# Kernel optimization log

Measured on AMD Instinct MI355X. Metric: run time of the kernel, lower is better.

The kernel has to match this reference:

```python
import jax, jax.numpy as jnp
import numpy as np

N = 100000      # nodes
E = 3200000     # edges
F_IN = 128      # dataset.num_features
H = 64          # hidden_channels
H2 = 32         # hidden_channels_2 (H//2); hidden_channels_3 unused by the module
C5 = 256        # 2 * num_features
NC = 6          # num_classes


def setup_inputs() -> dict:
    key = jax.random.key(0)
    ks = jax.random.split(key, 24)

    def w(k, fi, fo):
        return jax.random.normal(k, (fi, fo), jnp.float32) / np.float32(np.sqrt(fi))

    inp = {
        "x": jax.random.normal(ks[0], (N, F_IN), jnp.float32),
        "edge_index": jax.random.randint(ks[1], (2, E), 0, N, dtype=jnp.int32),
        "batch": jnp.zeros((N,), jnp.int32),
        # GCNConv weights/biases (conv_i: x @ W then normalized aggregation + b)
        "W1": w(ks[2], F_IN, H),  "b1": jnp.zeros((H,), jnp.float32),
        "W2": w(ks[3], H, H),     "b2": jnp.zeros((H,), jnp.float32),
        "W3": w(ks[4], H, H2),    "b3": jnp.zeros((H2,), jnp.float32),
        "W4": w(ks[5], H2, H2),   "b4": jnp.zeros((H2,), jnp.float32),
        "W5": w(ks[6], H2, C5),   "b5": jnp.zeros((C5,), jnp.float32),
        # Linear layers
        "Wl1": w(ks[7], C5, 24),  "bl1": jnp.zeros((24,), jnp.float32),
        "Wl2": w(ks[8], 24, 18),  "bl2": jnp.zeros((18,), jnp.float32),
        "Wl3": w(ks[9], 18, 12),  "bl3": jnp.zeros((12,), jnp.float32),
        "Wc":  w(ks[10], 24, NC), "bc": jnp.zeros((NC,), jnp.float32),
    }
    return inp


def reference(x, edge_index, batch,
              W1, b1, W2, b2, W3, b3, W4, b4, W5, b5,
              Wl1, bl1, Wl2, bl2, Wl3, bl3, Wc, bc):
    # --- GCN normalization (PyG GCNConv: add self loops, sym norm) ---
    loops = jnp.arange(N, dtype=edge_index.dtype)
    src = jnp.concatenate([edge_index[0], loops])   # message sources (x_j)
    dst = jnp.concatenate([edge_index[1], loops])   # aggregation targets
    deg = jax.ops.segment_sum(jnp.ones_like(dst, jnp.float32), dst, num_segments=N)
    dinv = jnp.where(deg > 0, jax.lax.rsqrt(jnp.maximum(deg, 1.0)), 0.0)
    norm = (dinv[src] * dinv[dst])[:, None]         # [E+N, 1]

    def gcn(h, W, b):
        m = (h @ W)[src] * norm
        return jax.ops.segment_sum(m, dst, num_segments=N) + b

    h = jnp.tanh(gcn(x, W1, b1))
    h = jnp.tanh(gcn(h, W2, b2))
    h = jnp.tanh(gcn(h, W3, b3))
    h = jnp.tanh(gcn(h, W4, b4))
    h = jnp.tanh(gcn(h, W5, b5))
    h = jnp.tanh(h @ Wl1 + bl1)
    h = jnp.tanh(h @ Wl2 + bl2)
    h = jnp.tanh(h @ Wl3 + bl3)                      # [N, 12]
    e = jnp.concatenate([h[edge_index[0]], h[edge_index[1]]], axis=1)  # [E, 24]
    out = e @ Wc + bc                                # [E, NC]
    return (out, e)
```

## Files before the change

### kernel.cpp

```cpp
#include <hip/hip_runtime.h>

constexpr int BKT_SHIFT = 7;
constexpr int NBKT_PAD  = 1024;
constexpr int CHUNK     = 8192;
constexpr int MAXSEG    = 6144;

__global__ __launch_bounds__(256) void k1_hist(const int* __restrict__ dst,
                                               int* __restrict__ Hist, int ne) {
    __shared__ int lh[NBKT_PAD];
    for (int i = threadIdx.x; i < NBKT_PAD; i += 256) lh[i] = 0;
    __syncthreads();
    int base = blockIdx.x * CHUNK;
    int lim = min(CHUNK, ne - base);
    for (int i = threadIdx.x; i < lim; i += 256)
        atomicAdd(&lh[dst[base + i] >> BKT_SHIFT], 1);
    __syncthreads();
    for (int i = threadIdx.x; i < NBKT_PAD; i += 256)
        Hist[(size_t)blockIdx.x * NBKT_PAD + i] = lh[i];
}

__global__ __launch_bounds__(1024) void k2_scan(int* __restrict__ Hist,
                                                int* __restrict__ bktBase,
                                                int* __restrict__ row_ptrN, int nblk) {
    __shared__ int wsums[16];
    int t = threadIdx.x, wave = t >> 6, lane = t & 63;
    int tot = 0;
    for (int blk = 0; blk < nblk; ++blk) tot += Hist[(size_t)blk * NBKT_PAD + t];
    int x = tot;
    #pragma unroll
    for (int off = 1; off < 64; off <<= 1) {
        int y = __shfl_up(x, off, 64);
        if (lane >= off) x += y;
    }
    if (lane == 63) wsums[wave] = x;
    __syncthreads();
    if (t < 16) {
        int w = wsums[t];
        #pragma unroll
        for (int off = 1; off < 16; off <<= 1) {
            int y = __shfl_up(w, off, 64);
            if (t >= off) w += y;
        }
        wsums[t] = w;
    }
    __syncthreads();
    int excl = (wave ? wsums[wave - 1] : 0) + (x - tot);
    bktBase[t] = excl;
    if (t == 1023) { bktBase[1024] = excl + tot; *row_ptrN = excl + tot; }
    int run = excl;
    for (int blk = 0; blk < nblk; ++blk) {
        size_t idx = (size_t)blk * NBKT_PAD + t;
        int v = Hist[idx];
        Hist[idx] = run;
        run += v;
    }
}

__global__ __launch_bounds__(256) void k3_partition(const int* __restrict__ src,
                                                    const int* __restrict__ dst,
                                                    const int* __restrict__ Hist,
                                                    int* __restrict__ srcS,
                                                    int* __restrict__ dstS, int ne) {
    __shared__ int cur[NBKT_PAD];
    for (int i = threadIdx.x; i < NBKT_PAD; i += 256)
        cur[i] = Hist[(size_t)blockIdx.x * NBKT_PAD + i];
    __syncthreads();
    int base = blockIdx.x * CHUNK;
    int lim = min(CHUNK, ne - base);
    for (int i = threadIdx.x; i < lim; i += 256) {
        int d = dst[base + i];
        int s = src[base + i];
        int pos = atomicAdd(&cur[d >> BKT_SHIFT], 1);
        srcS[pos] = s;
        dstS[pos] = d;
    }
}

__global__ __launch_bounds__(256) void k4_csr(const int* __restrict__ srcS,
                                              const int* __restrict__ dstS,
                                              const int* __restrict__ bktBase,
                                              int* __restrict__ col_idx,
                                              int* __restrict__ row_ptr,
                                              float* __restrict__ dinv, int n) {
    __shared__ int hist[128];
    __shared__ int rbase[128];
    __shared__ int cur[128];
    __shared__ int stage[MAXSEG];
    int b = blockIdx.x;
    int segs = bktBase[b], sege = bktBase[b + 1];
    int seglen = sege - segs;
    int node0 = b << BKT_SHIFT;
    int nloc = min(128, n - node0);
    int t = threadIdx.x;
    if (t < 128) hist[t] = 0;
    __syncthreads();
    for (int i = t; i < seglen; i += 256)
        atomicAdd(&hist[dstS[segs + i] - node0], 1);
    __syncthreads();
    if (t < 64) {
        int a0 = hist[2 * t], a1 = hist[2 * t + 1];
        int pair = a0 + a1;
        int x = pair;
        #pragma unroll
        for (int off = 1; off < 64; off <<= 1) {
            int y = __shfl_up(x, off, 64);
            if (t >= off) x += y;
        }
        int excl = x - pair;
        rbase[2 * t] = excl;       rbase[2 * t + 1] = excl + a0;
        cur[2 * t]   = excl;       cur[2 * t + 1]   = excl + a0;
    }
    __syncthreads();
    if (seglen <= MAXSEG) {
        for (int i = t; i < seglen; i += 256) {
            int d = dstS[segs + i] - node0;
            int pos = atomicAdd(&cur[d], 1);
            stage[pos] = srcS[segs + i];
        }
        __syncthreads();
        for (int i = t; i < seglen; i += 256)
            col_idx[segs + i] = stage[i];
    } else {
        for (int i = t; i < seglen; i += 256) {
            int d = dstS[segs + i] - node0;
            int pos = atomicAdd(&cur[d], 1);
            col_idx[segs + pos] = srcS[segs + i];
        }
    }
    if (t < nloc) {
        row_ptr[node0 + t] = segs + rbase[t];
        dinv[node0 + t] = 1.0f / sqrtf((float)(hist[t] + 1));
    }
}

template<int K, int FOUT, int EPI, int RT>
__global__ __launch_bounds__(256) void gemm_tiled(const float* __restrict__ X,
        const float* __restrict__ W, const float* __restrict__ bias,
        const float* __restrict__ dinv, float* __restrict__ Y, int nrows) {
    __shared__ float Wl[K * FOUT];
    __shared__ float Xs[RT * K];
    int tid = threadIdx.x;
    const float4* Wg4 = (const float4*)W;
    float4* Wl4 = (float4*)Wl;
    for (int i = tid; i < K * FOUT / 4; i += 256) Wl4[i] = Wg4[i];
    int row0 = blockIdx.x * RT;
    int nr = min(RT, nrows - row0);
    if constexpr ((K & 3) == 0) {
        const float4* Xg4 = (const float4*)(X + (size_t)row0 * K);
        float4* Xs4 = (float4*)Xs;
        int lim = nr * (K / 4);
        for (int i = tid; i < lim; i += 256) Xs4[i] = Xg4[i];
    } else {
        const float* Xg = X + (size_t)row0 * K;
        int lim = nr * K;
        for (int i = tid; i < lim; i += 256) Xs[i] = Xg[i];
    }
    __syncthreads();

    if constexpr (FOUT == 256 || FOUT == 64 || FOUT == 32) {
        constexpr int NG  = 256 / FOUT;
        constexpr int RPT = RT / NG;
        int c = tid & (FOUT - 1);
        int g = tid / FOUT;
        int rbase = g * RPT;
        float acc[RPT];
        #pragma unroll
        for (int i = 0; i < RPT; ++i) acc[i] = 0.f;
        #pragma unroll 4
        for (int k = 0; k < K; ++k) {
            float wv = Wl[k * FOUT + c];
            #pragma unroll
            for (int i = 0; i < RPT; ++i)
                acc[i] = fmaf(Xs[(rbase + i) * K + k], wv, acc[i]);
        }
        float bv = (EPI == 1) ? bias[c] : 0.f;
        #pragma unroll
        for (int i = 0; i < RPT; ++i) {
            int r = row0 + rbase + i;
            if (r < nrows) {
                float v = acc[i];
                if (EPI == 0) v *= dinv[r];
                else          v = tanhf(v + bv);
                Y[(size_t)r * FOUT + c] = v;
            }
        }
    } else {
        constexpr int TOT = RT * FOUT;
        for (int o = tid; o < TOT; o += 256) {
            int r = o / FOUT;
            int c = o - r * FOUT;
            if (r >= nr) break;
            float acc = 0.f;
            #pragma unroll 4
            for (int k = 0; k < K; ++k)
                acc = fmaf(Xs[r * K + k], Wl[k * FOUT + c], acc);
            int rg = row0 + r;
            float v;
            if (EPI == 0) v = acc * dinv[rg];
            else          v = tanhf(acc + bias[c]);
            Y[(size_t)rg * FOUT + c] = v;
        }
    }
}

template<int F, bool FINAL>
__global__ __launch_bounds__(256) void aggregate_kernel(const float* __restrict__ Z,
        const int* __restrict__ row_ptr, const int* __restrict__ col_idx,
        const float* __restrict__ dinv, const float* __restrict__ bias,
        float* __restrict__ out, int n) {
    constexpr int LPR = F / 4;
    constexpr int G   = 64 / LPR;
    int tid = threadIdx.x;
    int wave = tid >> 6, lane = tid & 63;
    int g = lane / LPR;
    int c = lane - g * LPR;
    int node = blockIdx.x * 4 + wave;
    if (node >= n) return;
    int start = row_ptr[node];
    int end   = row_ptr[node + 1];
    float4 acc = make_float4(0.f, 0.f, 0.f, 0.f);
    int wbase = start;
    int iv = (wbase + lane < end) ? col_idx[wbase + lane] : 0;
    #pragma unroll 2
    for (int base = start; base < end; base += G) {
        if (base - wbase == 64) {
            wbase += 64;
            iv = (wbase + lane < end) ? col_idx[wbase + lane] : 0;
        }
        int s = __shfl(iv, (base - wbase) + g, 64);
        if (base + g < end) {
            const float4 v = *(const float4*)(Z + (size_t)s * F + c * 4);
            acc.x += v.x; acc.y += v.y; acc.z += v.z; acc.w += v.w;
        }
    }
    #pragma unroll
    for (int off = LPR; off < 64; off <<= 1) {
        acc.x += __shfl_xor(acc.x, off, 64);
        acc.y += __shfl_xor(acc.y, off, 64);
        acc.z += __shfl_xor(acc.z, off, 64);
        acc.w += __shfl_xor(acc.w, off, 64);
    }
    if (g == 0) {
        const float4 sv = *(const float4*)(Z + (size_t)node * F + c * 4);
        float di = dinv[node];
        float4 r;
        r.x = di * (acc.x + sv.x);
        r.y = di * (acc.y + sv.y);
        r.z = di * (acc.z + sv.z);
        r.w = di * (acc.w + sv.w);
        if (FINAL) {
            const float4 bv = *(const float4*)(bias + c * 4);
            r.x = tanhf(r.x + bv.x);
            r.y = tanhf(r.y + bv.y);
            r.z = tanhf(r.z + bv.z);
            r.w = tanhf(r.w + bv.w);
        }
        *(float4*)(out + (size_t)node * F + c * 4) = r;
    }
}

__global__ __launch_bounds__(256) void mul_dinv_kernel(const float* __restrict__ h,
        const float* __restrict__ dinv, float* __restrict__ Z, int total, int shift) {
    int idx = blockIdx.x * 256 + threadIdx.x;
    if (idx < total) Z[idx] = h[idx] * dinv[idx >> shift];
}

__global__ __launch_bounds__(256) void edge_kernel(const int* __restrict__ src,
        const int* __restrict__ dst, const float* __restrict__ h,
        const float* __restrict__ Wc, const float* __restrict__ bc,
        float* __restrict__ out, float* __restrict__ efeat, int ne) {
    __shared__ float Wl[144];
    __shared__ float bl[6];
    if (threadIdx.x < 144) Wl[threadIdx.x] = Wc[threadIdx.x];
    if (threadIdx.x < 6) bl[threadIdx.x] = bc[threadIdx.x];
    __syncthreads();
    int e = blockIdx.x * 256 + threadIdx.x;
    if (e >= ne) return;
    int s = src[e], d = dst[e];
    const float4* hs4 = (const float4*)(h + (size_t)s * 12);
    const float4* hd4 = (const float4*)(h + (size_t)d * 12);
    float4 v0 = hs4[0], v1 = hs4[1], v2 = hs4[2];
    float4 v3 = hd4[0], v4 = hd4[1], v5 = hd4[2];
    float v[24];
    ((float4*)v)[0] = v0; ((float4*)v)[1] = v1; ((float4*)v)[2] = v2;
    ((float4*)v)[3] = v3; ((float4*)v)[4] = v4; ((float4*)v)[5] = v5;
    float4* ef4 = (float4*)(efeat + (size_t)e * 24);
    ef4[0] = v0; ef4[1] = v1; ef4[2] = v2; ef4[3] = v3; ef4[4] = v4; ef4[5] = v5;
    float o[6];
    #pragma unroll
    for (int c = 0; c < 6; ++c) {
        float acc = bl[c];
        #pragma unroll
        for (int k = 0; k < 24; ++k) acc = fmaf(v[k], Wl[k * 6 + c], acc);
        o[c] = acc;
    }
    float2* o2 = (float2*)(out + (size_t)e * 6);
    o2[0] = make_float2(o[0], o[1]);
    o2[1] = make_float2(o[2], o[3]);
    o2[2] = make_float2(o[4], o[5]);
}

extern "C" void kernel_launch(void* const* d_in, const int* in_sizes, int n_in,
                              void* d_out, int out_size, void* d_ws, size_t ws_size,
                              hipStream_t stream) {
    const int N = in_sizes[0] / 128;
    const int E = in_sizes[1] / 2;

    const float* x   = (const float*)d_in[0];
    const int*   ei  = (const int*)d_in[1];
    const int*   srcE = ei;
    const int*   dstE = ei + E;
    const float* W1 = (const float*)d_in[3];  const float* b1 = (const float*)d_in[4];
    const float* W2 = (const float*)d_in[5];  const float* b2 = (const float*)d_in[6];
    const float* W3 = (const float*)d_in[7];  const float* b3 = (const float*)d_in[8];
    const float* W4 = (const float*)d_in[9];  const float* b4 = (const float*)d_in[10];
    const float* W5 = (const float*)d_in[11]; const float* b5 = (const float*)d_in[12];
    const float* Wl1 = (const float*)d_in[13]; const float* bl1 = (const float*)d_in[14];
    const float* Wl2 = (const float*)d_in[15]; const float* bl2 = (const float*)d_in[16];
    const float* Wl3 = (const float*)d_in[17]; const float* bl3 = (const float*)d_in[18];
    const float* Wc  = (const float*)d_in[19]; const float* bc  = (const float*)d_in[20];

    char* ws = (char*)d_ws;
    size_t off = 0;
    auto take = [&](size_t bytes) -> char* {
        char* p = ws + off;
        off += (bytes + 255) & ~(size_t)255;
        return p;
    };
    int*   row_ptr = (int*)take((size_t)(N + 1) * 4);
    float* dinv    = (float*)take((size_t)N * 4);
    int*   col_idx = (int*)take((size_t)E * 4);
    float* h8      = (float*)take((size_t)N * 12 * 4);
    int*   bktBase = (int*)take((size_t)(NBKT_PAD + 1) * 4);

    float* outbuf  = (float*)d_out;
    float* eregion = outbuf + (size_t)E * 6;
    int* srcS = (int*)eregion;
    int* dstS = srcS + E;
    int* Hist = dstS + E;
    float* bufZ = eregion;
    float* bufH = eregion + (size_t)N * 64;
    float* bufC = eregion + (size_t)N * 128;

    int gE = (E + 255) / 256;
    int gAgg = (N + 3) / 4;
    int nblk = (E + CHUNK - 1) / CHUNK;
    int nbkt = (N + 127) >> BKT_SHIFT;
    auto tiles = [&](int rt) { return (N + rt - 1) / rt; };

    k1_hist<<<nblk, 256, 0, stream>>>(dstE, Hist, E);
    k2_scan<<<1, 1024, 0, stream>>>(Hist, bktBase, row_ptr + N, nblk);
    k3_partition<<<nblk, 256, 0, stream>>>(srcE, dstE, Hist, srcS, dstS, E);
    k4_csr<<<nbkt, 256, 0, stream>>>(srcS, dstS, bktBase, col_idx, row_ptr, dinv, N);

    gemm_tiled<128, 64, 0, 16><<<tiles(16), 256, 0, stream>>>(x, W1, nullptr, dinv, bufZ, N);
    aggregate_kernel<64, true><<<gAgg, 256, 0, stream>>>(bufZ, row_ptr, col_idx, dinv, b1, bufH, N);
    gemm_tiled<64, 64, 0, 16><<<tiles(16), 256, 0, stream>>>(bufH, W2, nullptr, dinv, bufZ, N);
    aggregate_kernel<64, true><<<gAgg, 256, 0, stream>>>(bufZ, row_ptr, col_idx, dinv, b2, bufH, N);
    gemm_tiled<64, 32, 0, 16><<<tiles(16), 256, 0, stream>>>(bufH, W3, nullptr, dinv, bufZ, N);
    aggregate_kernel<32, true><<<gAgg, 256, 0, stream>>>(bufZ, row_ptr, col_idx, dinv, b3, bufH, N);
    gemm_tiled<32, 32, 0, 16><<<tiles(16), 256, 0, stream>>>(bufH, W4, nullptr, dinv, bufZ, N);
    aggregate_kernel<32, true><<<gAgg, 256, 0, stream>>>(bufZ, row_ptr, col_idx, dinv, b4, bufH, N);
    mul_dinv_kernel<<<(N * 32 + 255) / 256, 256, 0, stream>>>(bufH, dinv, bufZ, N * 32, 5);
    aggregate_kernel<32, false><<<gAgg, 256, 0, stream>>>(bufZ, row_ptr, col_idx, dinv, nullptr, bufH, N);
    gemm_tiled<32, 256, 1, 16><<<tiles(16), 256, 0, stream>>>(bufH, W5, b5, nullptr, bufC, N);
    gemm_tiled<256, 24, 1, 16><<<tiles(16), 256, 0, stream>>>(bufC, Wl1, bl1, nullptr, bufZ, N);
    gemm_tiled<24, 18, 1, 64><<<tiles(64), 256, 0, stream>>>(bufZ, Wl2, bl2, nullptr, bufH, N);
    gemm_tiled<18, 12, 1, 64><<<tiles(64), 256, 0, stream>>>(bufH, Wl3, bl3, nullptr, h8, N);
    edge_kernel<<<gE, 256, 0, stream>>>(srcE, dstE, h8, Wc, bc, outbuf, eregion, E);
}
```

Before: 1.081 ms.

## Parallelize bucket scan, pack edge pairs, fuse MLP head, nontemporal edge stores

The single-block histogram scan becomes three kernels, so the per-bucket column sums and the offset rewrite run across several blocks. The partition step now writes packed int2 (src,dst) pairs, which halves the number of scattered stores. The dinv post-scale moves into the fourth aggregate's epilogue, removing the separate mul_dinv pass. The W5 GEMM and the three linear layers fuse into one head_kernel that keeps the 256-wide intermediate in shared memory instead of global memory. Edge-kernel outputs use nontemporal stores. The cost is higher shared-memory use in head_kernel (about 75KB), which may lower occupancy.

Result: slower. 1.455 ms (+34.5%).

```diff
diff --git a/kernel.cpp b/kernel.cpp
--- a/kernel.cpp
+++ b/kernel.cpp
@@ -1,4 +1,7 @@
 #include <hip/hip_runtime.h>
+
+typedef float f32x4 __attribute__((ext_vector_type(4)));
+typedef float f32x2 __attribute__((ext_vector_type(2)));
 
 constexpr int BKT_SHIFT = 7;
 constexpr int NBKT_PAD  = 1024;
@@ -19,13 +22,26 @@
         Hist[(size_t)blockIdx.x * NBKT_PAD + i] = lh[i];
 }
 
-__global__ __launch_bounds__(1024) void k2_scan(int* __restrict__ Hist,
-                                                int* __restrict__ bktBase,
-                                                int* __restrict__ row_ptrN, int nblk) {
+__global__ __launch_bounds__(128) void k2a_sum(const int* __restrict__ Hist,
+                                               int* __restrict__ bucketTot, int nblk) {
+    int b = blockIdx.x * 128 + threadIdx.x;
+    int tot = 0;
+    int blk = 0;
+    for (; blk + 4 <= nblk; blk += 4)
+        tot += Hist[(size_t)blk * NBKT_PAD + b] +
+               Hist[(size_t)(blk + 1) * NBKT_PAD + b] +
+               Hist[(size_t)(blk + 2) * NBKT_PAD + b] +
+               Hist[(size_t)(blk + 3) * NBKT_PAD + b];
+    for (; blk < nblk; ++blk) tot += Hist[(size_t)blk * NBKT_PAD + b];
+    bucketTot[b] = tot;
+}
+
+__global__ __launch_bounds__(1024) void k2b_scan(const int* __restrict__ bucketTot,
+                                                 int* __restrict__ bktBase,
+                                                 int* __restrict__ row_ptrN) {
     __shared__ int wsums[16];
     int t = threadIdx.x, wave = t >> 6, lane = t & 63;
-    int tot = 0;
-    for (int blk = 0; blk < nblk; ++blk) tot += Hist[(size_t)blk * NBKT_PAD + t];
+    int tot = bucketTot[t];
     int x = tot;
     #pragma unroll
     for (int off = 1; off < 64; off <<= 1) {
@@ -47,9 +63,14 @@
     int excl = (wave ? wsums[wave - 1] : 0) + (x - tot);
     bktBase[t] = excl;
     if (t == 1023) { bktBase[1024] = excl + tot; *row_ptrN = excl + tot; }
-    int run = excl;
+}
+
+__global__ __launch_bounds__(128) void k2c_rewrite(int* __restrict__ Hist,
+                                                   const int* __restrict__ bktBase, int nblk) {
+    int b = blockIdx.x * 128 + threadIdx.x;
+    int run = bktBase[b];
     for (int blk = 0; blk < nblk; ++blk) {
-        size_t idx = (size_t)blk * NBKT_PAD + t;
+        size_t idx = (size_t)blk * NBKT_PAD + b;
         int v = Hist[idx];
         Hist[idx] = run;
         run += v;
@@ -59,8 +80,7 @@
 __global__ __launch_bounds__(256) void k3_partition(const int* __restrict__ src,
                                                     const int* __restrict__ dst,
                                                     const int* __restrict__ Hist,
-                                                    int* __restrict__ srcS,
-                                                    int* __restrict__ dstS, int ne) {
+                                                    int2* __restrict__ es, int ne) {
     __shared__ int cur[NBKT_PAD];
     for (int i = threadIdx.x; i < NBKT_PAD; i += 256)
         cur[i] = Hist[(size_t)blockIdx.x * NBKT_PAD + i];
@@ -71,13 +91,11 @@
         int d = dst[base + i];
         int s = src[base + i];
         int pos = atomicAdd(&cur[d >> BKT_SHIFT], 1);
-        srcS[pos] = s;
-        dstS[pos] = d;
-    }
-}
-
-__global__ __launch_bounds__(256) void k4_csr(const int* __restrict__ srcS,
-                                              const int* __restrict__ dstS,
+        es[pos] = make_int2(s, d);
+    }
+}
+
+__global__ __launch_bounds__(256) void k4_csr(const int2* __restrict__ es,
                                               const int* __restrict__ bktBase,
                                               int* __restrict__ col_idx,
                                               int* __restrict__ row_ptr,
@@ -95,7 +113,7 @@
     if (t < 128) hist[t] = 0;
     __syncthreads();
     for (int i = t; i < seglen; i += 256)
-        atomicAdd(&hist[dstS[segs + i] - node0], 1);
+        atomicAdd(&hist[es[segs + i].y - node0], 1);
     __syncthreads();
     if (t < 64) {
         int a0 = hist[2 * t], a1 = hist[2 * t + 1];
@@ -113,18 +131,18 @@
     __syncthreads();
     if (seglen <= MAXSEG) {
         for (int i = t; i < seglen; i += 256) {
-            int d = dstS[segs + i] - node0;
-            int pos = atomicAdd(&cur[d], 1);
-            stage[pos] = srcS[segs + i];
+            int2 e = es[segs + i];
+            int pos = atomicAdd(&cur[e.y - node0], 1);
+            stage[pos] = e.x;
         }
         __syncthreads();
         for (int i = t; i < seglen; i += 256)
             col_idx[segs + i] = stage[i];
     } else {
         for (int i = t; i < seglen; i += 256) {
-            int d = dstS[segs + i] - node0;
-            int pos = atomicAdd(&cur[d], 1);
-            col_idx[segs + pos] = srcS[segs + i];
+            int2 e = es[segs + i];
+            int pos = atomicAdd(&cur[e.y - node0], 1);
+            col_idx[segs + pos] = e.x;
         }
     }
     if (t < nloc) {
@@ -145,65 +163,115 @@
     for (int i = tid; i < K * FOUT / 4; i += 256) Wl4[i] = Wg4[i];
     int row0 = blockIdx.x * RT;
     int nr = min(RT, nrows - row0);
-    if constexpr ((K & 3) == 0) {
+    {
         const float4* Xg4 = (const float4*)(X + (size_t)row0 * K);
         float4* Xs4 = (float4*)Xs;
         int lim = nr * (K / 4);
         for (int i = tid; i < lim; i += 256) Xs4[i] = Xg4[i];
-    } else {
-        const float* Xg = X + (size_t)row0 * K;
-        int lim = nr * K;
-        for (int i = tid; i < lim; i += 256) Xs[i] = Xg[i];
-    }
-    __syncthreads();
-
-    if constexpr (FOUT == 256 || FOUT == 64 || FOUT == 32) {
-        constexpr int NG  = 256 / FOUT;
-        constexpr int RPT = RT / NG;
-        int c = tid & (FOUT - 1);
-        int g = tid / FOUT;
-        int rbase = g * RPT;
-        float acc[RPT];
-        #pragma unroll
-        for (int i = 0; i < RPT; ++i) acc[i] = 0.f;
+    }
+    __syncthreads();
+
+    constexpr int NG  = 256 / FOUT;
+    constexpr int RPT = RT / NG;
+    int c = tid & (FOUT - 1);
+    int g = tid / FOUT;
+    int rbase = g * RPT;
+    float acc[RPT];
+    #pragma unroll
+    for (int i = 0; i < RPT; ++i) acc[i] = 0.f;
+    #pragma unroll 4
+    for (int k = 0; k < K; ++k) {
+        float wv = Wl[k * FOUT + c];
+        #pragma unroll
+        for (int i = 0; i < RPT; ++i)
+            acc[i] = fmaf(Xs[(rbase + i) * K + k], wv, acc[i]);
+    }
+    float bv = (EPI == 1) ? bias[c] : 0.f;
+    #pragma unroll
+    for (int i = 0; i < RPT; ++i) {
+        int r = row0 + rbase + i;
+        if (r < nrows) {
+            float v = acc[i];
+            if (EPI == 0) v *= dinv[r];
+            else          v = tanhf(v + bv);
+            Y[(size_t)r * FOUT + c] = v;
+        }
+    }
+}
+
+__global__ __launch_bounds__(256) void head_kernel(const float* __restrict__ X,
+        const float* __restrict__ W5, const float* __restrict__ b5,
+        const float* __restrict__ Wl1, const float* __restrict__ bl1,
+        const float* __restrict__ Wl2, const float* __restrict__ bl2,
+        const float* __restrict__ Wl3, const float* __restrict__ bl3,
+        float* __restrict__ Y, int nrows) {
+    constexpr int RT = 16;
+    __shared__ float W5s[32 * 256];
+    __shared__ float W1s[256 * 24];
+    __shared__ float W2s[24 * 18];
+    __shared__ float W3s[18 * 12];
+    __shared__ float b1s[24], b2s[18], b3s[12];
+    __shared__ float Xs[RT * 32];
+    __shared__ float H5[RT * 257];
+    __shared__ float H24[RT * 25];
+    __shared__ float H18[RT * 19];
+    int tid = threadIdx.x;
+    for (int i = tid; i < 32 * 256 / 4; i += 256) ((float4*)W5s)[i] = ((const float4*)W5)[i];
+    for (int i = tid; i < 256 * 24 / 4; i += 256) ((float4*)W1s)[i] = ((const float4*)Wl1)[i];
+    for (int i = tid; i < 432; i += 256) W2s[i] = Wl2[i];
+    for (int i = tid; i < 216; i += 256) W3s[i] = Wl3[i];
+    if (tid < 24) b1s[tid] = bl1[tid];
+    if (tid < 18) b2s[tid] = bl2[tid];
+    if (tid < 12) b3s[tid] = bl3[tid];
+    float b5r = b5[tid];
+    int row0 = blockIdx.x * RT;
+    int nr = min(RT, nrows - row0);
+    {
+        const float4* Xg4 = (const float4*)(X + (size_t)row0 * 32);
+        for (int i = tid; i < nr * 8; i += 256) ((float4*)Xs)[i] = Xg4[i];
+    }
+    __syncthreads();
+    {
+        float acc[RT];
+        #pragma unroll
+        for (int r = 0; r < RT; ++r) acc[r] = 0.f;
         #pragma unroll 4
-        for (int k = 0; k < K; ++k) {
-            float wv = Wl[k * FOUT + c];
+        for (int k = 0; k < 32; ++k) {
+            float wv = W5s[k * 256 + tid];
             #pragma unroll
-            for (int i = 0; i < RPT; ++i)
-                acc[i] = fmaf(Xs[(rbase + i) * K + k], wv, acc[i]);
-        }
-        float bv = (EPI == 1) ? bias[c] : 0.f;
-        #pragma unroll
-        for (int i = 0; i < RPT; ++i) {
-            int r = row0 + rbase + i;
-            if (r < nrows) {
-                float v = acc[i];
-                if (EPI == 0) v *= dinv[r];
-                else          v = tanhf(v + bv);
-                Y[(size_t)r * FOUT + c] = v;
-            }
-        }
-    } else {
-        constexpr int TOT = RT * FOUT;
-        for (int o = tid; o < TOT; o += 256) {
-            int r = o / FOUT;
-            int c = o - r * FOUT;
-            if (r >= nr) break;
-            float acc = 0.f;
-            #pragma unroll 4
-            for (int k = 0; k < K; ++k)
-                acc = fmaf(Xs[r * K + k], Wl[k * FOUT + c], acc);
-            int rg = row0 + r;
-            float v;
-            if (EPI == 0) v = acc * dinv[rg];
-            else          v = tanhf(acc + bias[c]);
-            Y[(size_t)rg * FOUT + c] = v;
-        }
-    }
-}
-
-template<int F, bool FINAL>
+            for (int r = 0; r < RT; ++r)
+                acc[r] = fmaf(Xs[r * 32 + k], wv, acc[r]);
+        }
+        #pragma unroll
+        for (int r = 0; r < RT; ++r) H5[r * 257 + tid] = tanhf(acc[r] + b5r);
+    }
+    __syncthreads();
+    for (int o = tid; o < RT * 24; o += 256) {
+        int r = o / 24, c = o - r * 24;
+        float acc = 0.f;
+        #pragma unroll 4
+        for (int k = 0; k < 256; ++k) acc = fmaf(H5[r * 257 + k], W1s[k * 24 + c], acc);
+        H24[r * 25 + c] = tanhf(acc + b1s[c]);
+    }
+    __syncthreads();
+    for (int o = tid; o < RT * 18; o += 256) {
+        int r = o / 18, c = o - r * 18;
+        float acc = 0.f;
+        #pragma unroll
+        for (int k = 0; k < 24; ++k) acc = fmaf(H24[r * 25 + k], W2s[k * 18 + c], acc);
+        H18[r * 19 + c] = tanhf(acc + b2s[c]);
+    }
+    __syncthreads();
+    for (int o = tid; o < RT * 12; o += 256) {
+        int r = o / 12, c = o - r * 12;
+        float acc = 0.f;
+        #pragma unroll
+        for (int k = 0; k < 18; ++k) acc = fmaf(H18[r * 19 + k], W3s[k * 12 + c], acc);
+        if (r < nr) Y[(size_t)(row0 + r) * 12 + c] = tanhf(acc + b3s[c]);
+    }
+}
+
+template<int F, bool FINAL, bool POSTSCALE>
 __global__ __launch_bounds__(256) void aggregate_kernel(const float* __restrict__ Z,
         const int* __restrict__ row_ptr, const int* __restrict__ col_idx,
         const float* __restrict__ dinv, const float* __restrict__ bias,
@@ -255,14 +323,9 @@
             r.z = tanhf(r.z + bv.z);
             r.w = tanhf(r.w + bv.w);
         }
+        if (POSTSCALE) { r.x *= di; r.y *= di; r.z *= di; r.w *= di; }
         *(float4*)(out + (size_t)node * F + c * 4) = r;
     }
-}
-
-__global__ __launch_bounds__(256) void mul_dinv_kernel(const float* __restrict__ h,
-        const float* __restrict__ dinv, float* __restrict__ Z, int total, int shift) {
-    int idx = blockIdx.x * 256 + threadIdx.x;
-    if (idx < total) Z[idx] = h[idx] * dinv[idx >> shift];
 }
 
 __global__ __launch_bounds__(256) void edge_kernel(const int* __restrict__ src,
@@ -277,15 +340,24 @@
     int e = blockIdx.x * 256 + threadIdx.x;
     if (e >= ne) return;
     int s = src[e], d = dst[e];
-    const float4* hs4 = (const float4*)(h + (size_t)s * 12);
-    const float4* hd4 = (const float4*)(h + (size_t)d * 12);
-    float4 v0 = hs4[0], v1 = hs4[1], v2 = hs4[2];
-    float4 v3 = hd4[0], v4 = hd4[1], v5 = hd4[2];
+    const float* hs = h + (size_t)s * 12;
+    const float* hd = h + (size_t)d * 12;
+    f32x4 v0 = *(const f32x4*)(hs + 0);
+    f32x4 v1 = *(const f32x4*)(hs + 4);
+    f32x4 v2 = *(const f32x4*)(hs + 8);
+    f32x4 v3 = *(const f32x4*)(hd + 0);
+    f32x4 v4 = *(const f32x4*)(hd + 4);
+    f32x4 v5 = *(const f32x4*)(hd + 8);
     float v[24];
-    ((float4*)v)[0] = v0; ((float4*)v)[1] = v1; ((float4*)v)[2] = v2;
-    ((float4*)v)[3] = v3; ((float4*)v)[4] = v4; ((float4*)v)[5] = v5;
-    float4* ef4 = (float4*)(efeat + (size_t)e * 24);
-    ef4[0] = v0; ef4[1] = v1; ef4[2] = v2; ef4[3] = v3; ef4[4] = v4; ef4[5] = v5;
+    *(f32x4*)(v + 0)  = v0; *(f32x4*)(v + 4)  = v1; *(f32x4*)(v + 8)  = v2;
+    *(f32x4*)(v + 12) = v3; *(f32x4*)(v + 16) = v4; *(f32x4*)(v + 20) = v5;
+    f32x4* ef4 = (f32x4*)(efeat + (size_t)e * 24);
+    __builtin_nontemporal_store(v0, ef4 + 0);
+    __builtin_nontemporal_store(v1, ef4 + 1);
+    __builtin_nontemporal_store(v2, ef4 + 2);
+    __builtin_nontemporal_store(v3, ef4 + 3);
+    __builtin_nontemporal_store(v4, ef4 + 4);
+    __builtin_nontemporal_store(v5, ef4 + 5);
     float o[6];
     #pragma unroll
     for (int c = 0; c < 6; ++c) {
@@ -294,10 +366,13 @@
         for (int k = 0; k < 24; ++k) acc = fmaf(v[k], Wl[k * 6 + c], acc);
         o[c] = acc;
     }
-    float2* o2 = (float2*)(out + (size_t)e * 6);
-    o2[0] = make_float2(o[0], o[1]);
-    o2[1] = make_float2(o[2], o[3]);
-    o2[2] = make_float2(o[4], o[5]);
+    f32x2* o2 = (f32x2*)(out + (size_t)e * 6);
+    f32x2 p0; p0.x = o[0]; p0.y = o[1];
+    f32x2 p1; p1.x = o[2]; p1.y = o[3];
+    f32x2 p2; p2.x = o[4]; p2.y = o[5];
+    __builtin_nontemporal_store(p0, o2 + 0);
+    __builtin_nontemporal_store(p1, o2 + 1);
+    __builtin_nontemporal_store(p2, o2 + 2);
 }
 
 extern "C" void kernel_launch(void* const* d_in, const int* in_sizes, int n_in,
@@ -327,20 +402,19 @@
         off += (bytes + 255) & ~(size_t)255;
         return p;
     };
-    int*   row_ptr = (int*)take((size_t)(N + 1) * 4);
-    float* dinv    = (float*)take((size_t)N * 4);
-    int*   col_idx = (int*)take((size_t)E * 4);
-    float* h8      = (float*)take((size_t)N * 12 * 4);
-    int*   bktBase = (int*)take((size_t)(NBKT_PAD + 1) * 4);
+    int*   row_ptr   = (int*)take((size_t)(N + 1) * 4);
+    float* dinv      = (float*)take((size_t)N * 4);
+    int*   col_idx   = (int*)take((size_t)E * 4);
+    float* h8        = (float*)take((size_t)N * 12 * 4);
+    int*   bktBase   = (int*)take((size_t)(NBKT_PAD + 1) * 4);
+    int*   bucketTot = (int*)take((size_t)NBKT_PAD * 4);
 
     float* outbuf  = (float*)d_out;
     float* eregion = outbuf + (size_t)E * 6;
-    int* srcS = (int*)eregion;
-    int* dstS = srcS + E;
-    int* Hist = dstS + E;
+    int2* es  = (int2*)eregion;
+    int*  Hist = (int*)(es + E);
     float* bufZ = eregion;
     float* bufH = eregion + (size_t)N * 64;
-    float* bufC = eregion + (size_t)N * 128;
 
     int gE = (E + 255) / 256;
     int gAgg = (N + 3) / 4;
@@ -349,23 +423,21 @@
     auto tiles = [&](int rt) { return (N + rt - 1) / rt; };
 
     k1_hist<<<nblk, 256, 0, stream>>>(dstE, Hist, E);
-    k2_scan<<<1, 1024, 0, stream>>>(Hist, bktBase, row_ptr + N, nblk);
-    k3_partition<<<nblk, 256, 0, stream>>>(srcE, dstE, Hist, srcS, dstS, E);
-    k4_csr<<<nbkt, 256, 0, stream>>>(srcS, dstS, bktBase, col_idx, row_ptr, dinv, N);
+    k2a_sum<<<NBKT_PAD / 128, 128, 0, stream>>>(Hist, bucketTot, nblk);
+    k2b_scan<<<1, 1024, 0, stream>>>(bucketTot, bktBase, row_ptr + N);
+    k2c_rewrite<<<NBKT_PAD / 128, 128, 0, stream>>>(Hist, bktBase, nblk);
+    k3_partition<<<nblk, 256, 0, stream>>>(srcE, dstE, Hist, es, E);
+    k4_csr<<<nbkt, 256, 0, stream>>>(es, bktBase, col_idx, row_ptr, dinv, N);
 
     gemm_tiled<128, 64, 0, 16><<<tiles(16), 256, 0, stream>>>(x, W1, nullptr, dinv, bufZ, N);
-    aggregate_kernel<64, true><<<gAgg, 256, 0, stream>>>(bufZ, row_ptr, col_idx, dinv, b1, bufH, N);
+    aggregate_kernel<64, true, false><<<gAgg, 256, 0, stream>>>(bufZ, row_ptr, col_idx, dinv, b1, bufH, N);
     gemm_tiled<64, 64, 0, 16><<<tiles(16), 256, 0, stream>>>(bufH, W2, nullptr, dinv, bufZ, N);
-    aggregate_kernel<64, true><<<gAgg, 256, 0, stream>>>(bufZ, row_ptr, col_idx, dinv, b2, bufH, N);
+    aggregate_kernel<64, true, false><<<gAgg, 256, 0, stream>>>(bufZ, row_ptr, col_idx, dinv, b2, bufH, N);
     gemm_tiled<64, 32, 0, 16><<<tiles(16), 256, 0, stream>>>(bufH, W3, nullptr, dinv, bufZ, N);
-    aggregate_kernel<32, true><<<gAgg, 256, 0, stream>>>(bufZ, row_ptr, col_idx, dinv, b3, bufH, N);
+    aggregate_kernel<32, true, false><<<gAgg, 256, 0, stream>>>(bufZ, row_ptr, col_idx, dinv, b3, bufH, N);
     gemm_tiled<32, 32, 0, 16><<<tiles(16), 256, 0, stream>>>(bufH, W4, nullptr, dinv, bufZ, N);
-    aggregate_kernel<32, true><<<gAgg, 256, 0, stream>>>(bufZ, row_ptr, col_idx, dinv, b4, bufH, N);
-    mul_dinv_kernel<<<(N * 32 + 255) / 256, 256, 0, stream>>>(bufH, dinv, bufZ, N * 32, 5);
-    aggregate_kernel<32, false><<<gAgg, 256, 0, stream>>>(bufZ, row_ptr, col_idx, dinv, nullptr, bufH, N);
-    gemm_tiled<32, 256, 1, 16><<<tiles(16), 256, 0, stream>>>(bufH, W5, b5, nullptr, bufC, N);
-    gemm_tiled<256, 24, 1, 16><<<tiles(16), 256, 0, stream>>>(bufC, Wl1, bl1, nullptr, bufZ, N);
-    gemm_tiled<24, 18, 1, 64><<<tiles(64), 256, 0, stream>>>(bufZ, Wl2, bl2, nullptr, bufH, N);
-    gemm_tiled<18, 12, 1, 64><<<tiles(64), 256, 0, stream>>>(bufH, Wl3, bl3, nullptr, h8, N);
+    aggregate_kernel<32, true, true><<<gAgg, 256, 0, stream>>>(bufZ, row_ptr, col_idx, dinv, b4, bufH, N);
+    aggregate_kernel<32, false, false><<<gAgg, 256, 0, stream>>>(bufH, row_ptr, col_idx, dinv, nullptr, bufZ, N);
+    head_kernel<<<tiles(16), 256, 0, stream>>>(bufZ, W5, b5, Wl1, bl1, Wl2, bl2, Wl3, bl3, h8, N);
     edge_kernel<<<gE, 256, 0, stream>>>(srcE, dstE, h8, Wc, bc, outbuf, eregion, E);
 }
```
